# Kernel optimization log

Hardware: AMD Instinct MI355X
Metric: run time of the kernel (lower is better)

Reference implementation:

```python
import jax, jax.numpy as jnp
import numpy as np

N = 20000          # nodes
E = 320000         # edges (avg degree 16)
C0, C1, C2 = 128, 64, 32   # multiplicities of 0e,1e,2e in node embedding (dim 480)
FC = 64            # edge scalar feature dim (fc_neurons[0])
WN = 3 * C0        # depthwise TP weight numel for nonzero paths
AVG_AGG = 16.0
LN_EPS = 1e-5


def setup_inputs() -> dict:
    key = jax.random.key(0)
    ks = jax.random.split(key, 20)
    inp = {
        'node_input':   jax.random.normal(ks[0], (N, 480), jnp.float32),
        'edge_attr':    jax.random.normal(ks[1], (E, 9), jnp.float32),   # sh lmax=2
        'edge_scalars': jax.random.normal(ks[2], (E, FC), jnp.float32),
        'edge_src':     jax.random.randint(ks[3], (E,), 0, N),
        'edge_dst':     jax.random.randint(ks[4], (E,), 0, N),
        'batch':        jnp.zeros((N,), jnp.int32),
        # exp: LinearRS 1x0e -> 128x0e (bias on scalars)
        'exp_w':  jax.random.normal(ks[5], (C0,), jnp.float32),
        'exp_b':  jax.random.normal(ks[6], (C0,), jnp.float32) * 0.1,
        # radial MLP: 64 -> 64 (LN, SiLU) -> 384
        'rad_w1': jax.random.normal(ks[7], (FC, FC), jnp.float32) / np.sqrt(FC),
        'rad_b1': jnp.zeros((FC,), jnp.float32),
        'rad_gamma': jnp.ones((FC,), jnp.float32),
        'rad_beta':  jnp.zeros((FC,), jnp.float32),
        'rad_w2': jax.random.normal(ks[8], (FC, WN), jnp.float32) / np.sqrt(FC),
        'rad_b2': jnp.zeros((WN,), jnp.float32),
        'proj_w0': jax.random.normal(ks[9], (C0, C0), jnp.float32) / np.sqrt(C0),
        'proj_b0': jnp.zeros((C0,), jnp.float32),
        'proj_w1': jax.random.normal(ks[10], (C0, C1), jnp.float32) / np.sqrt(C0),
        'proj_w2': jax.random.normal(ks[11], (C0, C2), jnp.float32) / np.sqrt(C0),
    }
    return inp


def reference(node_input, edge_attr, edge_scalars, edge_src, edge_dst, batch,
              exp_w, exp_b, rad_w1, rad_b1, rad_gamma, rad_beta, rad_w2, rad_b2,
              proj_w0, proj_b0, proj_w1, proj_w2):
    n = node_input.shape[0]
    # exp: ones -> 128x0e scalars (l>0 outputs of a scalar->irreps linear are zero)
    ones = jnp.ones_like(node_input[:, :1])            # [N,1]
    node_scal = ones * exp_w[None, :] + exp_b          # [N,128]
    # radial profile: Linear -> LayerNorm -> SiLU -> Linear
    h = edge_scalars @ rad_w1 + rad_b1
    mu = h.mean(-1, keepdims=True)
    var = h.var(-1, keepdims=True)
    h = (h - mu) * jax.lax.rsqrt(var + LN_EPS) * rad_gamma + rad_beta
    h = jax.nn.silu(h)
    w = (h @ rad_w2 + rad_b2).reshape(-1, 3, C0)       # [E,3,128] per-path dw weights
    # gather source node scalars
    s = node_scal[edge_src]                            # [E,128]
    sh0 = edge_attr[:, 0:1]                            # [E,1]
    sh1 = edge_attr[:, 1:4]                            # [E,3]
    sh2 = edge_attr[:, 4:9]                            # [E,5]
    # depthwise tensor product: 0e (x) l -> l (CG is identity up to norm)
    out0 = (s * w[:, 0]) * sh0                         # [E,128]
    out1 = (s * w[:, 1])[:, :, None] * sh1[:, None, :] # [E,128,3]
    out2 = (s * w[:, 2])[:, :, None] * sh2[:, None, :] # [E,128,5]
    # equivariant projection per degree
    y0 = out0 @ proj_w0 + proj_b0                      # [E,128]
    y1 = jnp.einsum('ecm,cd->edm', out1, proj_w1)      # [E,64,3]
    y2 = jnp.einsum('ecm,cd->edm', out2, proj_w2)      # [E,32,5]
    y = jnp.concatenate([y0, y1.reshape(-1, C1 * 3), y2.reshape(-1, C2 * 5)], axis=-1)  # [E,480]
    # scaled scatter-add to destination nodes
    agg = jax.ops.segment_sum(y, edge_dst, num_segments=n)
    return agg / jnp.sqrt(jnp.asarray(AVG_AGG, y.dtype))
```

## Files before the change

kernel.cpp:

```cpp
#include <hip/hip_runtime.h>

#define FCn 64
#define LDP 68
#define TEB 64
#define GJK 576
#define ABP 12

__device__ __forceinline__ float silu_f(float x) { return x / (1.f + __expf(-x)); }

__global__ __launch_bounds__(256) void precomp_kernel(
    const float* __restrict__ exp_w, const float* __restrict__ exp_b,
    const float* __restrict__ rad_w2, const float* __restrict__ rad_b2,
    const float* __restrict__ proj_w0, const float* __restrict__ proj_b0,
    const float* __restrict__ proj_w1, const float* __restrict__ proj_w2,
    float* __restrict__ MT, float* __restrict__ cvec, float* __restrict__ b0s)
{
    const int r = blockIdx.x;
    const int c = threadIdx.x;
    const float* wrow = (r < FCn) ? (rad_w2 + (long long)r * 384) : rad_b2;
    float acc = 0.f;
    if (c < 128) {
        for (int q = 0; q < 128; ++q)
            acc += wrow[q] * (exp_w[q] + exp_b[q]) * proj_w0[q * 128 + c];
    } else if (c < 192) {
        const int d = c - 128;
        for (int q = 0; q < 128; ++q)
            acc += wrow[128 + q] * (exp_w[q] + exp_b[q]) * proj_w1[q * 64 + d];
    } else if (c < 224) {
        const int d = c - 192;
        for (int q = 0; q < 128; ++q)
            acc += wrow[256 + q] * (exp_w[q] + exp_b[q]) * proj_w2[q * 32 + d];
    }
    acc *= 0.25f;
    if (r < FCn) {
        if (c < 224) MT[c * FCn + r] = acc;
    } else {
        cvec[c] = acc;
        if (c < 128) b0s[c] = 0.25f * proj_b0[c];
    }
}

__global__ __launch_bounds__(256) void hist_kernel(const int* __restrict__ dst, int* __restrict__ cnt, int E)
{
    for (int e = blockIdx.x * 256 + threadIdx.x; e < E; e += gridDim.x * 256)
        atomicAdd(&cnt[dst[e]], 1);
}

__global__ __launch_bounds__(256) void scan_kernel(const int* __restrict__ cnt, int* __restrict__ off,
                                                   int* __restrict__ cur, int Nn, int Etot)
{
    __shared__ int part[256];
    __shared__ int spart[257];
    const int t = threadIdx.x;
    const int per = (Nn + 255) / 256;
    int s = 0;
    for (int i = 0; i < per; ++i) {
        const int idx = t * per + i;
        if (idx < Nn) s += cnt[idx];
    }
    part[t] = s;
    __syncthreads();
    if (t == 0) {
        int run = 0;
        spart[0] = 0;
        for (int i = 0; i < 256; ++i) { run += part[i]; spart[i + 1] = run; }
    }
    __syncthreads();
    int run = spart[t];
    for (int i = 0; i < per; ++i) {
        const int idx = t * per + i;
        if (idx < Nn) { off[idx] = run; cur[idx] = run; run += cnt[idx]; }
    }
    if (t == 0) off[Nn] = Etot;
}

__global__ __launch_bounds__(256) void scatter_kernel(const int* __restrict__ dst, int* __restrict__ cur,
                                                      int* __restrict__ eids, int E)
{
    for (int e = blockIdx.x * 256 + threadIdx.x; e < E; e += gridDim.x * 256) {
        const int pos = atomicAdd(&cur[dst[e]], 1);
        eids[pos] = e;
    }
}

__global__ __launch_bounds__(256, 4) void accumG_kernel(
    const float* __restrict__ edge_attr,
    const float* __restrict__ edge_scalars,
    const int*   __restrict__ eids,
    const int*   __restrict__ edge_dst,
    const float* __restrict__ rad_w1,
    const float* __restrict__ rad_b1,
    const float* __restrict__ rad_gamma,
    const float* __restrict__ rad_beta,
    float* __restrict__ G,
    float* __restrict__ Ab,
    int E)
{
    __shared__ float XT[FCn * LDP];
    __shared__ float Hb[TEB * LDP];
    __shared__ float Ea[TEB * ABP];
    __shared__ int   eids_l[TEB];
    __shared__ int   dst_l[TEB];
    const int t = threadIdx.x;
    const int p0 = blockIdx.x * TEB;

    if (t < TEB) {
        const int p = p0 + t;
        const int eid = (p < E) ? eids[p] : -1;
        eids_l[t] = eid;
        dst_l[t]  = (eid >= 0) ? edge_dst[eid] : -1;
    }
    __syncthreads();

    #pragma unroll
    for (int i = 0; i < 4; ++i) {
        const int idx = i * 256 + t;
        const int e  = idx >> 4;
        const int kq = idx & 15;
        const int eid = eids_l[e];
        float4 v = make_float4(0.f, 0.f, 0.f, 0.f);
        if (eid >= 0) v = *(const float4*)(edge_scalars + (long long)eid * FCn + kq * 4);
        XT[(kq * 4 + 0) * LDP + e] = v.x;
        XT[(kq * 4 + 1) * LDP + e] = v.y;
        XT[(kq * 4 + 2) * LDP + e] = v.z;
        XT[(kq * 4 + 3) * LDP + e] = v.w;
    }
    for (int i = t; i < TEB * 9; i += 256) {
        const int e = i / 9, j = i - e * 9;
        const int eid = eids_l[e];
        Ea[e * ABP + j] = (eid >= 0) ? edge_attr[(long long)eid * 9 + j] : 0.f;
    }
    __syncthreads();

    {
        const int eg = t >> 4, cg = t & 15;
        float a[4][4];
        #pragma unroll
        for (int i = 0; i < 4; ++i)
            #pragma unroll
            for (int j = 0; j < 4; ++j) a[i][j] = 0.f;
        for (int k = 0; k < FCn; ++k) {
            const float4 xv = *(const float4*)&XT[k * LDP + eg * 4];
            const float4 wv = *(const float4*)&rad_w1[k * FCn + cg * 4];
            const float xe[4] = {xv.x, xv.y, xv.z, xv.w};
            const float wc[4] = {wv.x, wv.y, wv.z, wv.w};
            #pragma unroll
            for (int i = 0; i < 4; ++i)
                #pragma unroll
                for (int j = 0; j < 4; ++j)
                    a[i][j] += xe[i] * wc[j];
        }
        const float4 bv = *(const float4*)&rad_b1[cg * 4];
        const float bb[4] = {bv.x, bv.y, bv.z, bv.w};
        #pragma unroll
        for (int i = 0; i < 4; ++i) {
            float4 o;
            o.x = a[i][0] + bb[0]; o.y = a[i][1] + bb[1];
            o.z = a[i][2] + bb[2]; o.w = a[i][3] + bb[3];
            *(float4*)&Hb[(eg * 4 + i) * LDP + cg * 4] = o;
        }
    }
    __syncthreads();

    {
        const int e = t >> 2, q4 = t & 3;
        const float* hrow = &Hb[e * LDP + q4 * 16];
        float4 r[4];
        float s1 = 0.f, s2 = 0.f;
        #pragma unroll
        for (int i = 0; i < 4; ++i) {
            r[i] = *(const float4*)(hrow + i * 4);
            s1 += r[i].x + r[i].y + r[i].z + r[i].w;
            s2 += r[i].x * r[i].x + r[i].y * r[i].y + r[i].z * r[i].z + r[i].w * r[i].w;
        }
        s1 += __shfl_xor(s1, 1); s1 += __shfl_xor(s1, 2);
        s2 += __shfl_xor(s2, 1); s2 += __shfl_xor(s2, 2);
        const float mu  = s1 * (1.f / 64.f);
        const float var = s2 * (1.f / 64.f) - mu * mu;
        const float rs  = rsqrtf(var + 1e-5f);
        #pragma unroll
        for (int i = 0; i < 4; ++i) {
            const int c0 = q4 * 16 + i * 4;
            const float4 gm = *(const float4*)&rad_gamma[c0];
            const float4 bt = *(const float4*)&rad_beta[c0];
            float4 o;
            o.x = silu_f((r[i].x - mu) * rs * gm.x + bt.x);
            o.y = silu_f((r[i].y - mu) * rs * gm.y + bt.y);
            o.z = silu_f((r[i].z - mu) * rs * gm.z + bt.z);
            o.w = silu_f((r[i].w - mu) * rs * gm.w + bt.w);
            *(float4*)&XT[e * LDP + c0] = o;
        }
    }
    __syncthreads();

    const int k  = t & 63;
    const int jg = t >> 6;
    const int j0 = jg, j1 = jg + 4;
    const bool has2 = (jg == 0);
    float g0 = 0.f, g1 = 0.f, g2 = 0.f;
    float a0 = 0.f, a1 = 0.f, a2 = 0.f;
    int curn = dst_l[0];
    for (int e = 0; e < TEB; ++e) {
        const int nid = dst_l[e];
        if (nid != curn) {
            if (curn >= 0) {
                float* gp = G + (long long)curn * GJK;
                atomicAdd(gp + j0 * 64 + k, g0);
                atomicAdd(gp + j1 * 64 + k, g1);
                if (has2) atomicAdd(gp + 8 * 64 + k, g2);
                if (k == 0) {
                    float* ap = Ab + (long long)curn * ABP;
                    atomicAdd(ap + j0, a0);
                    atomicAdd(ap + j1, a1);
                    if (has2) atomicAdd(ap + 8, a2);
                }
            }
            g0 = g1 = g2 = 0.f; a0 = a1 = a2 = 0.f;
            curn = nid;
        }
        if (nid < 0) break;
        const float h  = XT[e * LDP + k];
        const float e0 = Ea[e * ABP + j0];
        const float e1 = Ea[e * ABP + j1];
        g0 = fmaf(e0, h, g0); a0 += e0;
        g1 = fmaf(e1, h, g1); a1 += e1;
        if (has2) {
            const float e2 = Ea[e * ABP + 8];
            g2 = fmaf(e2, h, g2); a2 += e2;
        }
    }
    if (curn >= 0) {
        float* gp = G + (long long)curn * GJK;
        atomicAdd(gp + j0 * 64 + k, g0);
        atomicAdd(gp + j1 * 64 + k, g1);
        if (has2) atomicAdd(gp + 8 * 64 + k, g2);
        if (k == 0) {
            float* ap = Ab + (long long)curn * ABP;
            atomicAdd(ap + j0, a0);
            atomicAdd(ap + j1, a1);
            if (has2) atomicAdd(ap + 8, a2);
        }
    }
}

__global__ __launch_bounds__(512, 2) void project_kernel(
    const float* __restrict__ G, const float* __restrict__ Ab,
    const int*   __restrict__ off,
    const float* __restrict__ MT, const float* __restrict__ cvec,
    const float* __restrict__ b0s,
    float* __restrict__ out, int Nn)
{
    __shared__ float MTl[224 * LDP];
    __shared__ float Gs[4 * 9 * 72];
    __shared__ float sA[4 * ABP];
    __shared__ float cv[224];
    __shared__ float bs[128];
    __shared__ int   dg[4];
    const int t = threadIdx.x;

    for (int i = t; i < 224 * FCn; i += 512) {
        const int c = i >> 6, kk = i & 63;
        MTl[c * LDP + kk] = MT[i];
    }
    if (t < 224) cv[t] = cvec[t];
    if (t < 128) bs[t] = b0s[t];

    int tIdx = 0, jIdx = 0;
    if (t < 128)      { tIdx = t; jIdx = 0; }
    else if (t < 320) { const int idx = t - 128; tIdx = 128 + idx / 3; jIdx = 1 + idx % 3; }
    else if (t < 480) { const int idx = t - 320; tIdx = 192 + idx / 5; jIdx = 4 + idx % 5; }

    for (int n0 = blockIdx.x * 4; n0 < Nn; n0 += gridDim.x * 4) {
        for (int i = t; i < 4 * GJK; i += 512) {
            const int nb = i / GJK, r = i - nb * GJK;
            const int n = n0 + nb;
            Gs[nb * 648 + (r >> 6) * 72 + (r & 63)] = (n < Nn) ? G[(long long)n * GJK + r] : 0.f;
        }
        if (t < 4 * ABP) {
            const int nb = t / ABP, j = t - nb * ABP;
            const int n = n0 + nb;
            sA[t] = (n < Nn) ? Ab[(long long)n * ABP + j] : 0.f;
        }
        if (t < 4) {
            const int n = n0 + t;
            dg[t] = (n < Nn) ? off[n + 1] - off[n] : 0;
        }
        __syncthreads();
        if (t < 480) {
            const float cvv = cv[tIdx];
            const float bsv = (t < 128) ? bs[t] : 0.f;
            float acc0 = sA[0 * ABP + jIdx] * cvv + (float)dg[0] * bsv;
            float acc1 = sA[1 * ABP + jIdx] * cvv + (float)dg[1] * bsv;
            float acc2 = sA[2 * ABP + jIdx] * cvv + (float)dg[2] * bsv;
            float acc3 = sA[3 * ABP + jIdx] * cvv + (float)dg[3] * bsv;
            const float* mrow = &MTl[tIdx * LDP];
            const float* g0p = &Gs[0 * 648 + jIdx * 72];
            const float* g1p = &Gs[1 * 648 + jIdx * 72];
            const float* g2p = &Gs[2 * 648 + jIdx * 72];
            const float* g3p = &Gs[3 * 648 + jIdx * 72];
            #pragma unroll
            for (int q = 0; q < 16; ++q) {
                const float4 m  = *(const float4*)(mrow + q * 4);
                const float4 ga = *(const float4*)(g0p + q * 4);
                const float4 gb = *(const float4*)(g1p + q * 4);
                const float4 gc = *(const float4*)(g2p + q * 4);
                const float4 gd = *(const float4*)(g3p + q * 4);
                acc0 += m.x * ga.x + m.y * ga.y + m.z * ga.z + m.w * ga.w;
                acc1 += m.x * gb.x + m.y * gb.y + m.z * gb.z + m.w * gb.w;
                acc2 += m.x * gc.x + m.y * gc.y + m.z * gc.z + m.w * gc.w;
                acc3 += m.x * gd.x + m.y * gd.y + m.z * gd.z + m.w * gd.w;
            }
            const long long ob = (long long)n0 * 480 + t;
            if (n0 + 0 < Nn) out[ob           ] = acc0;
            if (n0 + 1 < Nn) out[ob + 480     ] = acc1;
            if (n0 + 2 < Nn) out[ob + 2 * 480 ] = acc2;
            if (n0 + 3 < Nn) out[ob + 3 * 480 ] = acc3;
        }
        __syncthreads();
    }
}

extern "C" void kernel_launch(void* const* d_in, const int* in_sizes, int n_in,
                              void* d_out, int out_size, void* d_ws, size_t ws_size,
                              hipStream_t stream)
{
    const float* edge_attr    = (const float*)d_in[1];
    const float* edge_scalars = (const float*)d_in[2];
    const int*   edge_dst     = (const int*)d_in[4];
    const float* exp_w     = (const float*)d_in[6];
    const float* exp_b     = (const float*)d_in[7];
    const float* rad_w1    = (const float*)d_in[8];
    const float* rad_b1    = (const float*)d_in[9];
    const float* rad_gamma = (const float*)d_in[10];
    const float* rad_beta  = (const float*)d_in[11];
    const float* rad_w2    = (const float*)d_in[12];
    const float* rad_b2    = (const float*)d_in[13];
    const float* proj_w0   = (const float*)d_in[14];
    const float* proj_b0   = (const float*)d_in[15];
    const float* proj_w1   = (const float*)d_in[16];
    const float* proj_w2   = (const float*)d_in[17];
    float* out = (float*)d_out;
    const int E = in_sizes[4];
    const int Nn = out_size / 480;

    float* MT   = (float*)d_ws;
    float* cvec = MT + 224 * FCn;
    float* b0s  = cvec + 256;
    int* off  = (int*)(b0s + 128);
    int* cnt  = off + (Nn + 1);
    int* cur  = cnt + Nn;
    int* eids = cur + Nn;
    size_t gOff = (size_t)((char*)(eids + E) - (char*)d_ws);
    gOff = (gOff + 255) & ~(size_t)255;
    float* G  = (float*)((char*)d_ws + gOff);
    float* Ab = G + (size_t)Nn * GJK;

    precomp_kernel<<<FCn + 1, 256, 0, stream>>>(exp_w, exp_b, rad_w2, rad_b2,
                                                proj_w0, proj_b0, proj_w1, proj_w2,
                                                MT, cvec, b0s);
    hipMemsetAsync(cnt, 0, (size_t)Nn * sizeof(int), stream);
    hipMemsetAsync(G, 0, (size_t)Nn * (GJK + ABP) * sizeof(float), stream);
    hist_kernel<<<512, 256, 0, stream>>>(edge_dst, cnt, E);
    scan_kernel<<<1, 256, 0, stream>>>(cnt, off, cur, Nn, E);
    scatter_kernel<<<512, 256, 0, stream>>>(edge_dst, cur, eids, E);

    const int blocks = (E + TEB - 1) / TEB;
    accumG_kernel<<<blocks, 256, 0, stream>>>(edge_attr, edge_scalars, eids, edge_dst,
                                              rad_w1, rad_b1, rad_gamma, rad_beta,
                                              G, Ab, E);
    project_kernel<<<512, 512, 0, stream>>>(G, Ab, off, MT, cvec, b0s, out, Nn);
}
```

Before: 542.1 us.

## Fuse zeroing into precomp, register-resident LayerNorm, and batch eight nodes in projection

Replaces the two memsets with extra blocks in the precompute kernel that zero G/Ab and the degree counts, removing separate launches. In accumG, the LayerNorm statistics are now computed from the GEMM registers with shuffles instead of a shared-memory round trip, one shared buffer is dropped, and occupancy is raised to 7 blocks. The edge accumulation loop takes an unrolled fast path when four consecutive edges share a destination. The projection kernel keeps each thread's MT row in registers, handles eight nodes per iteration with vectorised loads, and raises its occupancy hint, which increases register pressure and risks spills.

```diff
diff --git a/kernel.cpp b/kernel.cpp
--- a/kernel.cpp
+++ b/kernel.cpp
@@ -5,6 +5,7 @@
 #define TEB 64
 #define GJK 576
 #define ABP 12
+#define ZBLK 512
 
 __device__ __forceinline__ float silu_f(float x) { return x / (1.f + __expf(-x)); }
 
@@ -13,8 +14,17 @@
     const float* __restrict__ rad_w2, const float* __restrict__ rad_b2,
     const float* __restrict__ proj_w0, const float* __restrict__ proj_b0,
     const float* __restrict__ proj_w1, const float* __restrict__ proj_w2,
-    float* __restrict__ MT, float* __restrict__ cvec, float* __restrict__ b0s)
-{
+    float* __restrict__ MT, float* __restrict__ cvec, float* __restrict__ b0s,
+    float* __restrict__ zbase, long long zf4, int* __restrict__ cnt, int Nn)
+{
+    if (blockIdx.x >= 65) {
+        const long long tid = (long long)(blockIdx.x - 65) * 256 + threadIdx.x;
+        const long long stride = (long long)ZBLK * 256;
+        float4 z = make_float4(0.f, 0.f, 0.f, 0.f);
+        for (long long i = tid; i < zf4; i += stride) ((float4*)zbase)[i] = z;
+        for (long long i = tid; i < Nn; i += stride) cnt[i] = 0;
+        return;
+    }
     const int r = blockIdx.x;
     const int c = threadIdx.x;
     const float* wrow = (r < FCn) ? (rad_w2 + (long long)r * 384) : rad_b2;
@@ -54,6 +64,7 @@
     const int t = threadIdx.x;
     const int per = (Nn + 255) / 256;
     int s = 0;
+    #pragma unroll 8
     for (int i = 0; i < per; ++i) {
         const int idx = t * per + i;
         if (idx < Nn) s += cnt[idx];
@@ -67,6 +78,7 @@
     }
     __syncthreads();
     int run = spart[t];
+    #pragma unroll 8
     for (int i = 0; i < per; ++i) {
         const int idx = t * per + i;
         if (idx < Nn) { off[idx] = run; cur[idx] = run; run += cnt[idx]; }
@@ -83,7 +95,7 @@
     }
 }
 
-__global__ __launch_bounds__(256, 4) void accumG_kernel(
+__global__ __launch_bounds__(256, 7) void accumG_kernel(
     const float* __restrict__ edge_attr,
     const float* __restrict__ edge_scalars,
     const int*   __restrict__ eids,
@@ -97,9 +109,7 @@
     int E)
 {
     __shared__ float XT[FCn * LDP];
-    __shared__ float Hb[TEB * LDP];
     __shared__ float Ea[TEB * ABP];
-    __shared__ int   eids_l[TEB];
     __shared__ int   dst_l[TEB];
     const int t = threadIdx.x;
     const int p0 = blockIdx.x * TEB;
@@ -107,17 +117,16 @@
     if (t < TEB) {
         const int p = p0 + t;
         const int eid = (p < E) ? eids[p] : -1;
-        eids_l[t] = eid;
-        dst_l[t]  = (eid >= 0) ? edge_dst[eid] : -1;
-    }
-    __syncthreads();
+        dst_l[t] = (eid >= 0) ? edge_dst[eid] : -1;
+    }
 
     #pragma unroll
     for (int i = 0; i < 4; ++i) {
         const int idx = i * 256 + t;
         const int e  = idx >> 4;
         const int kq = idx & 15;
-        const int eid = eids_l[e];
+        const int p  = p0 + e;
+        const int eid = (p < E) ? eids[p] : -1;
         float4 v = make_float4(0.f, 0.f, 0.f, 0.f);
         if (eid >= 0) v = *(const float4*)(edge_scalars + (long long)eid * FCn + kq * 4);
         XT[(kq * 4 + 0) * LDP + e] = v.x;
@@ -127,68 +136,72 @@
     }
     for (int i = t; i < TEB * 9; i += 256) {
         const int e = i / 9, j = i - e * 9;
-        const int eid = eids_l[e];
+        const int p = p0 + e;
+        const int eid = (p < E) ? eids[p] : -1;
         Ea[e * ABP + j] = (eid >= 0) ? edge_attr[(long long)eid * 9 + j] : 0.f;
     }
     __syncthreads();
 
+    const int eg = t >> 4, cg = t & 15;
+    float a[4][4];
+    #pragma unroll
+    for (int i = 0; i < 4; ++i)
+        #pragma unroll
+        for (int j = 0; j < 4; ++j) a[i][j] = 0.f;
+    for (int k = 0; k < FCn; ++k) {
+        const float4 xv = *(const float4*)&XT[k * LDP + eg * 4];
+        const float4 wv = *(const float4*)&rad_w1[k * FCn + cg * 4];
+        const float xe[4] = {xv.x, xv.y, xv.z, xv.w};
+        const float wc[4] = {wv.x, wv.y, wv.z, wv.w};
+        #pragma unroll
+        for (int i = 0; i < 4; ++i)
+            #pragma unroll
+            for (int j = 0; j < 4; ++j)
+                a[i][j] += xe[i] * wc[j];
+    }
     {
-        const int eg = t >> 4, cg = t & 15;
-        float a[4][4];
-        #pragma unroll
-        for (int i = 0; i < 4; ++i)
-            #pragma unroll
-            for (int j = 0; j < 4; ++j) a[i][j] = 0.f;
-        for (int k = 0; k < FCn; ++k) {
-            const float4 xv = *(const float4*)&XT[k * LDP + eg * 4];
-            const float4 wv = *(const float4*)&rad_w1[k * FCn + cg * 4];
-            const float xe[4] = {xv.x, xv.y, xv.z, xv.w};
-            const float wc[4] = {wv.x, wv.y, wv.z, wv.w};
-            #pragma unroll
-            for (int i = 0; i < 4; ++i)
-                #pragma unroll
-                for (int j = 0; j < 4; ++j)
-                    a[i][j] += xe[i] * wc[j];
-        }
         const float4 bv = *(const float4*)&rad_b1[cg * 4];
         const float bb[4] = {bv.x, bv.y, bv.z, bv.w};
         #pragma unroll
+        for (int i = 0; i < 4; ++i)
+            #pragma unroll
+            for (int j = 0; j < 4; ++j) a[i][j] += bb[j];
+    }
+
+    float s1[4], s2[4];
+    #pragma unroll
+    for (int i = 0; i < 4; ++i) {
+        s1[i] = a[i][0] + a[i][1] + a[i][2] + a[i][3];
+        s2[i] = a[i][0]*a[i][0] + a[i][1]*a[i][1] + a[i][2]*a[i][2] + a[i][3]*a[i][3];
+    }
+    #pragma unroll
+    for (int m = 1; m < 16; m <<= 1) {
+        #pragma unroll
         for (int i = 0; i < 4; ++i) {
-            float4 o;
-            o.x = a[i][0] + bb[0]; o.y = a[i][1] + bb[1];
-            o.z = a[i][2] + bb[2]; o.w = a[i][3] + bb[3];
-            *(float4*)&Hb[(eg * 4 + i) * LDP + cg * 4] = o;
-        }
-    }
+            s1[i] += __shfl_xor(s1[i], m);
+            s2[i] += __shfl_xor(s2[i], m);
+        }
+    }
+
     __syncthreads();
 
     {
-        const int e = t >> 2, q4 = t & 3;
-        const float* hrow = &Hb[e * LDP + q4 * 16];
-        float4 r[4];
-        float s1 = 0.f, s2 = 0.f;
+        const float4 gm = *(const float4*)&rad_gamma[cg * 4];
+        const float4 bt = *(const float4*)&rad_beta[cg * 4];
+        const float gv[4] = {gm.x, gm.y, gm.z, gm.w};
+        const float bv2[4] = {bt.x, bt.y, bt.z, bt.w};
         #pragma unroll
         for (int i = 0; i < 4; ++i) {
-            r[i] = *(const float4*)(hrow + i * 4);
-            s1 += r[i].x + r[i].y + r[i].z + r[i].w;
-            s2 += r[i].x * r[i].x + r[i].y * r[i].y + r[i].z * r[i].z + r[i].w * r[i].w;
-        }
-        s1 += __shfl_xor(s1, 1); s1 += __shfl_xor(s1, 2);
-        s2 += __shfl_xor(s2, 1); s2 += __shfl_xor(s2, 2);
-        const float mu  = s1 * (1.f / 64.f);
-        const float var = s2 * (1.f / 64.f) - mu * mu;
-        const float rs  = rsqrtf(var + 1e-5f);
-        #pragma unroll
-        for (int i = 0; i < 4; ++i) {
-            const int c0 = q4 * 16 + i * 4;
-            const float4 gm = *(const float4*)&rad_gamma[c0];
-            const float4 bt = *(const float4*)&rad_beta[c0];
-            float4 o;
-            o.x = silu_f((r[i].x - mu) * rs * gm.x + bt.x);
-            o.y = silu_f((r[i].y - mu) * rs * gm.y + bt.y);
-            o.z = silu_f((r[i].z - mu) * rs * gm.z + bt.z);
-            o.w = silu_f((r[i].w - mu) * rs * gm.w + bt.w);
-            *(float4*)&XT[e * LDP + c0] = o;
+            const float mu  = s1[i] * (1.f / 64.f);
+            const float var = s2[i] * (1.f / 64.f) - mu * mu;
+            const float rs  = rsqrtf(var + 1e-5f);
+            float o[4];
+            #pragma unroll
+            for (int j = 0; j < 4; ++j) {
+                const float x = (a[i][j] - mu) * rs * gv[j] + bv2[j];
+                o[j] = silu_f(x);
+            }
+            *(float4*)&XT[(eg * 4 + i) * LDP + cg * 4] = make_float4(o[0], o[1], o[2], o[3]);
         }
     }
     __syncthreads();
@@ -200,7 +213,8 @@
     float g0 = 0.f, g1 = 0.f, g2 = 0.f;
     float a0 = 0.f, a1 = 0.f, a2 = 0.f;
     int curn = dst_l[0];
-    for (int e = 0; e < TEB; ++e) {
+    int e = 0;
+    while (e < TEB) {
         const int nid = dst_l[e];
         if (nid != curn) {
             if (curn >= 0) {
@@ -219,14 +233,32 @@
             curn = nid;
         }
         if (nid < 0) break;
-        const float h  = XT[e * LDP + k];
-        const float e0 = Ea[e * ABP + j0];
-        const float e1 = Ea[e * ABP + j1];
-        g0 = fmaf(e0, h, g0); a0 += e0;
-        g1 = fmaf(e1, h, g1); a1 += e1;
-        if (has2) {
-            const float e2 = Ea[e * ABP + 8];
-            g2 = fmaf(e2, h, g2); a2 += e2;
+        if (e + 4 <= TEB && dst_l[e + 3] == nid) {
+            #pragma unroll
+            for (int u = 0; u < 4; ++u) {
+                const int eu = e + u;
+                const float h  = XT[eu * LDP + k];
+                const float e0 = Ea[eu * ABP + j0];
+                const float e1 = Ea[eu * ABP + j1];
+                g0 = fmaf(e0, h, g0); a0 += e0;
+                g1 = fmaf(e1, h, g1); a1 += e1;
+                if (has2) {
+                    const float e2 = Ea[eu * ABP + 8];
+                    g2 = fmaf(e2, h, g2); a2 += e2;
+                }
+            }
+            e += 4;
+        } else {
+            const float h  = XT[e * LDP + k];
+            const float e0 = Ea[e * ABP + j0];
+            const float e1 = Ea[e * ABP + j1];
+            g0 = fmaf(e0, h, g0); a0 += e0;
+            g1 = fmaf(e1, h, g1); a1 += e1;
+            if (has2) {
+                const float e2 = Ea[e * ABP + 8];
+                g2 = fmaf(e2, h, g2); a2 += e2;
+            }
+            e += 1;
         }
     }
     if (curn >= 0) {
@@ -243,78 +275,68 @@
     }
 }
 
-__global__ __launch_bounds__(512, 2) void project_kernel(
+__global__ __launch_bounds__(512, 4) void project_kernel(
     const float* __restrict__ G, const float* __restrict__ Ab,
     const int*   __restrict__ off,
     const float* __restrict__ MT, const float* __restrict__ cvec,
     const float* __restrict__ b0s,
     float* __restrict__ out, int Nn)
 {
-    __shared__ float MTl[224 * LDP];
-    __shared__ float Gs[4 * 9 * 72];
-    __shared__ float sA[4 * ABP];
-    __shared__ float cv[224];
-    __shared__ float bs[128];
-    __shared__ int   dg[4];
+    __shared__ float Gs[8 * GJK];
+    __shared__ float sA[8 * ABP];
+    __shared__ int   dg[8];
     const int t = threadIdx.x;
-
-    for (int i = t; i < 224 * FCn; i += 512) {
-        const int c = i >> 6, kk = i & 63;
-        MTl[c * LDP + kk] = MT[i];
-    }
-    if (t < 224) cv[t] = cvec[t];
-    if (t < 128) bs[t] = b0s[t];
 
     int tIdx = 0, jIdx = 0;
     if (t < 128)      { tIdx = t; jIdx = 0; }
     else if (t < 320) { const int idx = t - 128; tIdx = 128 + idx / 3; jIdx = 1 + idx % 3; }
     else if (t < 480) { const int idx = t - 320; tIdx = 192 + idx / 5; jIdx = 4 + idx % 5; }
 
-    for (int n0 = blockIdx.x * 4; n0 < Nn; n0 += gridDim.x * 4) {
-        for (int i = t; i < 4 * GJK; i += 512) {
-            const int nb = i / GJK, r = i - nb * GJK;
-            const int n = n0 + nb;
-            Gs[nb * 648 + (r >> 6) * 72 + (r & 63)] = (n < Nn) ? G[(long long)n * GJK + r] : 0.f;
-        }
-        if (t < 4 * ABP) {
+    float4 m[16];
+    {
+        const float* mrow = MT + tIdx * FCn;
+        #pragma unroll
+        for (int q = 0; q < 16; ++q) m[q] = *(const float4*)(mrow + q * 4);
+    }
+    const float cvv = cvec[tIdx];
+    const float bsv = (t < 128) ? b0s[t] : 0.f;
+
+    for (int n0 = blockIdx.x * 8; n0 < Nn; n0 += gridDim.x * 8) {
+        const int nvalid = min(8, Nn - n0);
+        const int nf4 = (nvalid * GJK) >> 2;
+        for (int i = t; i < nf4; i += 512)
+            ((float4*)Gs)[i] = *(const float4*)(G + (long long)n0 * GJK + i * 4);
+        if (t < 8 * ABP) {
             const int nb = t / ABP, j = t - nb * ABP;
             const int n = n0 + nb;
             sA[t] = (n < Nn) ? Ab[(long long)n * ABP + j] : 0.f;
         }
-        if (t < 4) {
+        if (t < 8) {
             const int n = n0 + t;
             dg[t] = (n < Nn) ? off[n + 1] - off[n] : 0;
         }
         __syncthreads();
+
+        float acc[8];
+        #pragma unroll
+        for (int nb = 0; nb < 8; ++nb)
+            acc[nb] = sA[nb * ABP + jIdx] * cvv + (float)dg[nb] * bsv;
+        const float* gbase = Gs + jIdx * 64;
+        #pragma unroll
+        for (int q = 0; q < 16; ++q) {
+            const float4 mq = m[q];
+            #pragma unroll
+            for (int nb = 0; nb < 8; ++nb) {
+                const float4 g = *(const float4*)(gbase + nb * GJK + q * 4);
+                acc[nb] += mq.x * g.x + mq.y * g.y + mq.z * g.z + mq.w * g.w;
+            }
+        }
         if (t < 480) {
-            const float cvv = cv[tIdx];
-            const float bsv = (t < 128) ? bs[t] : 0.f;
-            float acc0 = sA[0 * ABP + jIdx] * cvv + (float)dg[0] * bsv;
-            float acc1 = sA[1 * ABP + jIdx] * cvv + (float)dg[1] * bsv;
-            float acc2 = sA[2 * ABP + jIdx] * cvv + (float)dg[2] * bsv;
-            float acc3 = sA[3 * ABP + jIdx] * cvv + (float)dg[3] * bsv;
-            const float* mrow = &MTl[tIdx * LDP];
-            const float* g0p = &Gs[0 * 648 + jIdx * 72];
-            const float* g1p = &Gs[1 * 648 + jIdx * 72];
-            const float* g2p = &Gs[2 * 648 + jIdx * 72];
-            const float* g3p = &Gs[3 * 648 + jIdx * 72];
-            #pragma unroll
-            for (int q = 0; q < 16; ++q) {
-                const float4 m  = *(const float4*)(mrow + q * 4);
-                const float4 ga = *(const float4*)(g0p + q * 4);
-                const float4 gb = *(const float4*)(g1p + q * 4);
-                const float4 gc = *(const float4*)(g2p + q * 4);
-                const float4 gd = *(const float4*)(g3p + q * 4);
-                acc0 += m.x * ga.x + m.y * ga.y + m.z * ga.z + m.w * ga.w;
-                acc1 += m.x * gb.x + m.y * gb.y + m.z * gb.z + m.w * gb.w;
-                acc2 += m.x * gc.x + m.y * gc.y + m.z * gc.z + m.w * gc.w;
-                acc3 += m.x * gd.x + m.y * gd.y + m.z * gd.z + m.w * gd.w;
-            }
-            const long long ob = (long long)n0 * 480 + t;
-            if (n0 + 0 < Nn) out[ob           ] = acc0;
-            if (n0 + 1 < Nn) out[ob + 480     ] = acc1;
-            if (n0 + 2 < Nn) out[ob + 2 * 480 ] = acc2;
-            if (n0 + 3 < Nn) out[ob + 3 * 480 ] = acc3;
+            #pragma unroll
+            for (int nb = 0; nb < 8; ++nb) {
+                if (n0 + nb < Nn)
+                    out[(long long)(n0 + nb) * 480 + t] = acc[nb];
+            }
         }
         __syncthreads();
     }
@@ -355,11 +377,10 @@
     float* G  = (float*)((char*)d_ws + gOff);
     float* Ab = G + (size_t)Nn * GJK;
 
-    precomp_kernel<<<FCn + 1, 256, 0, stream>>>(exp_w, exp_b, rad_w2, rad_b2,
-                                                proj_w0, proj_b0, proj_w1, proj_w2,
-                                                MT, cvec, b0s);
-    hipMemsetAsync(cnt, 0, (size_t)Nn * sizeof(int), stream);
-    hipMemsetAsync(G, 0, (size_t)Nn * (GJK + ABP) * sizeof(float), stream);
+    const long long zf4 = ((long long)Nn * (GJK + ABP)) >> 2;
+    precomp_kernel<<<65 + ZBLK, 256, 0, stream>>>(exp_w, exp_b, rad_w2, rad_b2,
+                                                  proj_w0, proj_b0, proj_w1, proj_w2,
+                                                  MT, cvec, b0s, G, zf4, cnt, Nn);
     hist_kernel<<<512, 256, 0, stream>>>(edge_dst, cnt, E);
     scan_kernel<<<1, 256, 0, stream>>>(cnt, off, cur, Nn, E);
     scatter_kernel<<<512, 256, 0, stream>>>(edge_dst, cur, eids, E);
```

Result: slower. 1.213 ms (+123.7%).
